# Optimization experiments

Hardware: AMD Instinct MI355X
Metric: run time of the kernel (lower is better)

## Reference

```python
import jax, jax.numpy as jnp
import numpy as np
from jax import lax

STRIDE = 16
ANCHOR_BASE = 16
PRE_NMS = 6000
POST_NMS = 2000
NMS_THRESH = 0.7


def _generate_anchors(base_size=16, ratios=(0.5, 1.0, 2.0), scales=(8, 16, 32)):
    w = h = float(base_size)
    x_ctr = 0.5 * (w - 1)
    y_ctr = 0.5 * (h - 1)
    size = w * h
    anchors = []
    for r in ratios:
        ws = np.round(np.sqrt(size / r))
        hs = np.round(ws * r)
        for s in scales:
            wss, hss = ws * s, hs * s
            anchors.append([x_ctr - 0.5 * (wss - 1), y_ctr - 0.5 * (hss - 1),
                            x_ctr + 0.5 * (wss - 1), y_ctr + 0.5 * (hss - 1)])
    return np.array(anchors, dtype=np.float32)  # [9,4]


def _all_anchors(width, height, stride):
    base = _generate_anchors(ANCHOR_BASE)  # [A,4]
    sx = np.arange(width, dtype=np.float32) * stride
    gy, gx = np.meshgrid(np.arange(height, dtype=np.float32) * stride, sx, indexing='ij')
    shifts = np.stack([gx.ravel(), gy.ravel(), gx.ravel(), gy.ravel()], axis=1)  # [K,4] h-major
    return jnp.asarray((shifts[:, None, :] + base[None, :, :]).reshape(-1, 4))  # [K*A,4]


def setup_inputs() -> dict:
    key = jax.random.key(0)
    k1, k2 = jax.random.split(key)
    H = W = 64
    bbox_deltas = jax.random.normal(k1, (1, 36, H, W), dtype=jnp.float32)
    scores = jax.random.uniform(k2, (1, 2, 9 * H, W), dtype=jnp.float32)
    return {"bbox_deltas": bbox_deltas, "scores": scores, "im_w": 1024, "im_h": 1024}


def reference(bbox_deltas, scores, im_w, im_h):
    H, W = bbox_deltas.shape[2], bbox_deltas.shape[3]
    # fg scores: reshape [1,2,9H,W] -> [1,18,H,W], take channels 9:18
    sc = scores.reshape(1, 18, H, W)[:, 9:, :, :].transpose(0, 2, 3, 1).reshape(-1)
    dl = bbox_deltas.transpose(0, 2, 3, 1).reshape(-1, 4)
    anchors = _all_anchors(W, H, STRIDE)

    # bbox_transform_inv (decode)
    aw = anchors[:, 2] - anchors[:, 0] + 1.0
    ah = anchors[:, 3] - anchors[:, 1] + 1.0
    acx = anchors[:, 0] + 0.5 * aw
    acy = anchors[:, 1] + 0.5 * ah
    pcx = dl[:, 0] * aw + acx
    pcy = dl[:, 1] * ah + acy
    pw = jnp.exp(dl[:, 2]) * aw
    ph = jnp.exp(dl[:, 3]) * ah
    x1 = jnp.clip(pcx - 0.5 * pw, 0.0, im_w - 1.0)
    y1 = jnp.clip(pcy - 0.5 * ph, 0.0, im_h - 1.0)
    x2 = jnp.clip(pcx + 0.5 * pw, 0.0, im_w - 1.0)
    y2 = jnp.clip(pcy + 0.5 * ph, 0.0, im_h - 1.0)
    props = jnp.stack([x1, y1, x2, y2], axis=1)

    # min-size filter
    thresh = 16.0 * (float(im_h) / float(im_w))
    keep_f = ((x2 - x1 + 1.0) >= thresh) & ((y2 - y1 + 1.0) >= thresh)
    sc_m = jnp.where(keep_f, sc, -jnp.inf)

    # pre-NMS top-k by score
    top_sc, idx = lax.top_k(sc_m, PRE_NMS)
    top_p = props[idx]  # [PRE_NMS,4], sorted by score desc
    valid = jnp.isfinite(top_sc)

    # pairwise IoU (with +1 box convention, as in py_cpu_nms)
    bx1, by1, bx2, by2 = top_p[:, 0], top_p[:, 1], top_p[:, 2], top_p[:, 3]
    areas = (bx2 - bx1 + 1.0) * (by2 - by1 + 1.0)
    iw = jnp.maximum(jnp.minimum(bx2[:, None], bx2[None, :]) - jnp.maximum(bx1[:, None], bx1[None, :]) + 1.0, 0.0)
    ih = jnp.maximum(jnp.minimum(by2[:, None], by2[None, :]) - jnp.maximum(by1[:, None], by1[None, :]) + 1.0, 0.0)
    inter = iw * ih
    iou = inter / (areas[:, None] + areas[None, :] - inter)
    sup = iou > NMS_THRESH  # [N,N]

    ar = jnp.arange(PRE_NMS)

    def body(i, keep):
        row = sup[i] & keep[i] & (ar > i)
        return keep & (~row)

    keep = lax.fori_loop(0, PRE_NMS, body, valid)

    # take first POST_NMS kept (in score order), scatter into fixed-size output
    rank = jnp.cumsum(keep.astype(jnp.int32)) - 1
    sel = keep & (rank < POST_NMS)
    dst = jnp.where(sel, rank, POST_NMS)  # invalid rows dumped into slot POST_NMS
    out_b = jnp.zeros((POST_NMS + 1, 4), dtype=jnp.float32).at[dst].set(
        jnp.where(sel[:, None], top_p, 0.0))[:POST_NMS]
    out_s = jnp.zeros((POST_NMS + 1,), dtype=jnp.float32).at[dst].set(
        jnp.where(sel, top_sc, 0.0))[:POST_NMS]
    blob = jnp.concatenate([jnp.zeros((POST_NMS, 1), dtype=jnp.float32), out_b], axis=1)
    return blob, out_s[:, None]
```

## Files before the change

kernel.cpp:

```cpp
#include <hip/hip_runtime.h>
#include <math.h>

typedef unsigned int u32;
typedef unsigned long long u64;

#define NANCH   36864
#define PRE     6000
#define POST    2000
#define NWORDS  94
#define NSTEP   47
#define ROWSP   6016

#define OFF_PROPS   ((size_t)0)
#define OFF_SV      ((size_t)589824)
#define OFF_SORTED  ((size_t)884736)
#define OFF_SEL     ((size_t)932864)
#define OFF_MASKT   ((size_t)1227776)
#define OFF_CTRL    ((size_t)5751808)
#define OFF_H1      ((size_t)5752064)

__device__ __constant__ float BA[9][4] = {
  {-84.f,-40.f,99.f,55.f},   {-176.f,-88.f,191.f,103.f}, {-360.f,-184.f,375.f,199.f},
  {-56.f,-56.f,71.f,71.f},   {-120.f,-120.f,135.f,135.f},{-248.f,-248.f,263.f,263.f},
  {-36.f,-80.f,51.f,95.f},   {-80.f,-168.f,95.f,183.f},  {-168.f,-344.f,183.f,359.f}};

__device__ __forceinline__ u32 key_bin(u32 key) {
  if (key < 0xBF000000u) return 0u;
  u32 b = ((key >> 13) - 0x5F800u) + 1u;
  return b > 1024u ? 1024u : b;
}

__global__ void decode_k(const float* __restrict__ deltas, const float* __restrict__ scores,
                         const int* __restrict__ imw_p, const int* __restrict__ imh_p,
                         float4* __restrict__ props, u64* __restrict__ sortvals,
                         u32* __restrict__ h1, u32* __restrict__ ctrl) {
  #pragma clang fp contract(off)
  if (threadIdx.x == 0) ctrl[6] = 0u;
  int i = blockIdx.x * 256 + threadIdx.x;
  if (i >= NANCH) return;
  int a = i % 9;
  int pix = i / 9;
  int x = pix & 63, y = pix >> 6;

  float sc = scores[(9 + a) * 4096 + pix];
  float d0 = deltas[(a * 4 + 0) * 4096 + pix];
  float d1 = deltas[(a * 4 + 1) * 4096 + pix];
  float d2 = deltas[(a * 4 + 2) * 4096 + pix];
  float d3 = deltas[(a * 4 + 3) * 4096 + pix];

  float gx = (float)(x * 16), gy = (float)(y * 16);
  float ax1 = gx + BA[a][0], ay1 = gy + BA[a][1];
  float ax2 = gx + BA[a][2], ay2 = gy + BA[a][3];
  float aw = ax2 - ax1 + 1.0f, ah = ay2 - ay1 + 1.0f;
  float acx = ax1 + 0.5f * aw, acy = ay1 + 0.5f * ah;

  float pcx = d0 * aw + acx;
  float pcy = d1 * ah + acy;
  float pw = (float)exp((double)d2) * aw;
  float ph = (float)exp((double)d3) * ah;

  float imw1 = (float)imw_p[0] - 1.0f, imh1 = (float)imh_p[0] - 1.0f;
  float x1 = fminf(fmaxf(pcx - 0.5f * pw, 0.0f), imw1);
  float y1 = fminf(fmaxf(pcy - 0.5f * ph, 0.0f), imh1);
  float x2 = fminf(fmaxf(pcx + 0.5f * pw, 0.0f), imw1);
  float y2 = fminf(fmaxf(pcy + 0.5f * ph, 0.0f), imh1);
  props[i] = make_float4(x1, y1, x2, y2);

  float thresh = 16.0f * ((float)imh_p[0] / (float)imw_p[0]);
  bool keep = (x2 - x1 + 1.0f >= thresh) && (y2 - y1 + 1.0f >= thresh);
  u32 key = keep ? (__float_as_uint(sc) | 0x80000000u) : 0u;
  sortvals[i] = ((u64)key << 32) | (u64)(0xFFFFFFFFu - (u32)i);
  u32 bin = key_bin(key);
  if (bin) atomicAdd(&h1[bin], 1u);
}

__global__ void compact_k(const u64* __restrict__ sv, const u32* __restrict__ h1,
                          u32* __restrict__ ctrl, u64* __restrict__ sel) {
  __shared__ u32 Lchosen;
  int t = threadIdx.x;
  if (t < 64) {
    int l = t;
    u32 loc[16], suf[16];
    #pragma unroll
    for (int k = 0; k < 16; ++k) loc[k] = h1[1 + l * 16 + k];
    u32 acc = 0;
    #pragma unroll
    for (int k = 15; k >= 0; --k) { acc += loc[k]; suf[k] = acc; }
    u32 sfx = acc;
    for (int off = 1; off < 64; off <<= 1) {
      u32 o = __shfl_down(sfx, off);
      if (l + off < 64) sfx += o;
    }
    u32 S_above = sfx - acc;
    u64 mball = __ballot(suf[0] + S_above >= (u32)PRE);
    if (mball == 0ULL) { if (l == 0) Lchosen = 0u; }
    else {
      int L = 63 - __builtin_clzll(mball);
      if (l == L) {
        int kk = 0;
        for (int k = 15; k >= 0; --k)
          if (suf[k] + S_above >= (u32)PRE) { kk = k; break; }
        Lchosen = (u32)(1 + 16 * L + kk);
      }
    }
  }
  __syncthreads();
  u32 chosen = Lchosen;
  int i = blockIdx.x * 256 + t;
  if (i >= NANCH) return;
  u64 v = sv[i];
  if (key_bin((u32)(v >> 32)) >= chosen) {
    u32 p = atomicAdd(&ctrl[6], 1u);
    sel[p] = v;
  }
}

__global__ void rank_k(const u64* __restrict__ sel, const u32* __restrict__ ctrl,
                       u64* __restrict__ sorted) {
  __shared__ u64 sj[256];
  u32 n = ctrl[6];
  int i = blockIdx.x * 256 + threadIdx.x;
  if ((u32)(blockIdx.x * 256) >= n) return;
  u64 vi = ((u32)i < n) ? sel[i] : 0ULL;
  u32 cnt = 0;
  for (u32 jb = 0; jb < n; jb += 256) {
    __syncthreads();
    if (jb + threadIdx.x < n) sj[threadIdx.x] = sel[jb + threadIdx.x];
    __syncthreads();
    u32 m = min(256u, n - jb);
    #pragma unroll 8
    for (u32 j = 0; j < m; ++j) cnt += (u32)(sj[j] > vi);
  }
  if ((u32)i < n && cnt < (u32)PRE) sorted[cnt] = vi;
}

__global__ void mask_k(const u64* __restrict__ sorted, const float4* __restrict__ props,
                       u64* __restrict__ maskT) {
  #pragma clang fp contract(off)
  __shared__ float4 cb[64];
  int jb = blockIdx.x;
  if (jb < (int)blockIdx.y) return;
  int i = blockIdx.y * 64 + threadIdx.x;
  int jj = jb * 64 + threadIdx.x;
  float4 cc = make_float4(0.f, 0.f, 0.f, 0.f);
  if (jj < PRE) {
    u64 v = sorted[jj];
    cc = props[0xFFFFu - ((u32)v & 0xFFFFu)];
  }
  cb[threadIdx.x] = cc;
  __syncthreads();
  if (i >= PRE) return;
  u64 vi = sorted[i];
  float4 b = props[0xFFFFu - ((u32)vi & 0xFFFFu)];
  float ai = (b.z - b.x + 1.0f) * (b.w - b.y + 1.0f);
  u64 bits = 0ULL;
  int jmax = min(64, PRE - jb * 64);
  for (int j = 0; j < jmax; ++j) {
    float4 c = cb[j];
    float aj = (c.z - c.x + 1.0f) * (c.w - c.y + 1.0f);
    float iw = fmaxf(fminf(b.z, c.z) - fmaxf(b.x, c.x) + 1.0f, 0.0f);
    float ih = fmaxf(fminf(b.w, c.w) - fmaxf(b.y, c.y) + 1.0f, 0.0f);
    float inter = iw * ih;
    float iou = inter / (ai + aj - inter);
    bits |= ((u64)(iou > 0.7f)) << j;
  }
  maskT[(size_t)jb * ROWSP + i] = bits;
}

__device__ __forceinline__ u64 rl64(u64 v, int lane) {
  u32 lo = (u32)__builtin_amdgcn_readlane((int)(u32)v, lane);
  u32 hi = (u32)__builtin_amdgcn_readlane((int)(u32)(v >> 32), lane);
  return ((u64)hi << 32) | (u64)lo;
}

__global__ void __launch_bounds__(1024) nms_scan_k(const u64* __restrict__ maskT,
                                                   const u64* __restrict__ sorted,
                                                   const float4* __restrict__ props,
                                                   float* __restrict__ out) {
  __shared__ u64 Lrem[NWORDS];
  __shared__ u64 Ldiag[128][2];
  __shared__ u64 Lkb[NWORDS];
  __shared__ u64 LkA, LkB;
  __shared__ int Lstop;
  __shared__ u32 Lpre[NWORDS];
  const int t = threadIdx.x;
  const int g = t >> 7;
  const int w = t & 127;
  const bool loader = (w < NWORDS);
  u64 rv = 0;
  u64 B0[16], B1[16];
  int kept = 0;

#define ISSUE(bb, BUF) \
  if ((bb) < NSTEP && loader) { \
    const u64* p_ = maskT + (size_t)w * ROWSP + (bb) * 128 + g * 16; \
    _Pragma("unroll") \
    for (int k = 0; k < 16; ++k) BUF[k] = p_[k]; \
  }

  ISSUE(0, B0)
  ISSUE(1, B1)

  if (t < NWORDS) { Lrem[t] = 0ULL; Lkb[t] = 0ULL; }
  if (t == 0) Lstop = 0;
  __syncthreads();
  for (int r = t; r < PRE; r += 1024)
    if ((u32)(sorted[r] >> 32) == 0u)
      atomicOr((unsigned long long*)&Lrem[r >> 6], 1ULL << (r & 63));
  if (t == 0)
    atomicOr((unsigned long long*)&Lrem[NWORDS - 1],
             ~((1ULL << (PRE - (NWORDS - 1) * 64)) - 1ULL));
  __syncthreads();

#define STEP(bb, BUF) { \
    const int A_ = 2 * (bb), Bw_ = A_ + 1; \
    if (w == A_ || w == Bw_) {            \
      atomicOr((u32*)&Lrem[w], (u32)rv); \
      atomicOr(((u32*)&Lrem[w]) + 1, (u32)(rv >> 32)); \
      const int c_ = (w == Bw_); \
      _Pragma("unroll") \
      for (int k = 0; k < 16; ++k) { \
        int i_ = g * 16 + k; \
        if (c_ || i_ < 64) Ldiag[i_][c_] = BUF[k]; \
      } \
    } \
    __syncthreads();                      \
    if (t < 64) { \
      u64 a0 = Ldiag[t][0], b0 = Ldiag[t][1], b1 = Ldiag[64 + t][1]; \
      u64 availA = ~Lrem[A_]; \
      u64 availB = ~Lrem[Bw_]; \
      u64 kbA = 0, kbB = 0; \
      while (availA) { \
        int i_ = __builtin_ctzll(availA); \
        kbA |= 1ULL << i_; \
        availA &= ~rl64(a0, i_) & ~((2ULL << i_) - 1ULL);  \
        availB &= ~rl64(b0, i_); \
      } \
      while (availB) { \
        int i_ = __builtin_ctzll(availB); \
        kbB |= 1ULL << i_; \
        availB &= ~rl64(b1, i_) & ~((2ULL << i_) - 1ULL); \
      } \
      if (t == 0) { \
        Lkb[A_] = kbA; Lkb[Bw_] = kbB; LkA = kbA; LkB = kbB; \
        kept += (int)__popcll(kbA) + (int)__popcll(kbB); \
        if (kept >= POST) Lstop = 1; \
      } \
    } \
    __syncthreads();                      \
    { \
      u64 kA_ = LkA, kB_ = LkB; \
      _Pragma("unroll") \
      for (int k = 0; k < 16; ++k) { \
        int i_ = g * 16 + k; \
        u64 bit_ = (i_ < 64) ? (kA_ >> i_) : (kB_ >> (i_ - 64)); \
        rv |= (0ULL - (bit_ & 1ULL)) & BUF[k]; \
      } \
    } \
    ISSUE((bb) + 2, BUF)                  \
    if (Lstop) break; }

  for (int bb = 0; bb < NSTEP; bb += 2) {
    STEP(bb, B0)
    if (bb + 1 < NSTEP) STEP(bb + 1, B1)
  }
#undef ISSUE
#undef STEP

  __syncthreads();
  for (int i = t; i < 12000; i += 1024) out[i] = 0.0f;
  if (t == 0) {
    u32 run = 0;
    for (int w2 = 0; w2 < NWORDS; ++w2) { Lpre[w2] = run; run += (u32)__popcll(Lkb[w2]); }
  }
  __syncthreads();
  for (int i = t; i < PRE; i += 1024) {
    u64 word = Lkb[i >> 6];
    if ((word >> (i & 63)) & 1ULL) {
      u32 rank = Lpre[i >> 6] + (u32)__popcll(word & ((1ULL << (i & 63)) - 1ULL));
      if (rank < POST) {
        u64 v = sorted[i];
        float4 b = props[0xFFFFu - ((u32)v & 0xFFFFu)];
        out[rank * 5 + 1] = b.x;
        out[rank * 5 + 2] = b.y;
        out[rank * 5 + 3] = b.z;
        out[rank * 5 + 4] = b.w;
        out[10000 + rank] = __uint_as_float((u32)(v >> 32) & 0x7FFFFFFFu);
      }
    }
  }
}

extern "C" void kernel_launch(void* const* d_in, const int* in_sizes, int n_in,
                              void* d_out, int out_size, void* d_ws, size_t ws_size,
                              hipStream_t stream) {
  const float* deltas = (const float*)d_in[0];
  const float* scores = (const float*)d_in[1];
  const int* imw = (const int*)d_in[2];
  const int* imh = (const int*)d_in[3];
  char* ws = (char*)d_ws;

  float4* props   = (float4*)(ws + OFF_PROPS);
  u64*    svals   = (u64*)(ws + OFF_SV);
  u64*    sorted  = (u64*)(ws + OFF_SORTED);
  u64*    sel     = (u64*)(ws + OFF_SEL);
  u64*    maskT   = (u64*)(ws + OFF_MASKT);
  u32*    ctrl    = (u32*)(ws + OFF_CTRL);
  u32*    h1      = (u32*)(ws + OFF_H1);

  hipMemsetAsync(h1, 0, 1025 * sizeof(u32), stream);

  decode_k<<<144, 256, 0, stream>>>(deltas, scores, imw, imh, props, svals, h1, ctrl);
  compact_k<<<144, 256, 0, stream>>>(svals, h1, ctrl, sel);
  rank_k<<<144, 256, 0, stream>>>(sel, ctrl, sorted);

  dim3 mgrid(NWORDS, NWORDS);
  mask_k<<<mgrid, 64, 0, stream>>>(sorted, props, maskT);

  nms_scan_k<<<1, 1024, 0, stream>>>(maskT, sorted, props, (float*)d_out);
}
```

Baseline: 378.8 us.

## Restructure NMS scan to one word per step with a single barrier

The serial NMS scan now advances one 64-bit word per step instead of two. Every thread redundantly computes the keep-bits from a double-buffered diagonal block, so the shared broadcast of keep masks and the second barrier per step are gone. The next word's removal mask and diagonal are published by the owning loader thread, and later steps skip loads for words already processed (w >= bb). The trade-off is twice as many steps, each with a barrier, in exchange for fewer barriers per word and no serial single-thread bookkeeping.

```diff
diff --git a/kernel.cpp b/kernel.cpp
--- a/kernel.cpp
+++ b/kernel.cpp
@@ -8,7 +8,6 @@
 #define PRE     6000
 #define POST    2000
 #define NWORDS  94
-#define NSTEP   47
 #define ROWSP   6016
 
 #define OFF_PROPS   ((size_t)0)
@@ -178,31 +177,28 @@
                                                    const float4* __restrict__ props,
                                                    float* __restrict__ out) {
   __shared__ u64 Lrem[NWORDS];
-  __shared__ u64 Ldiag[128][2];
+  __shared__ u64 Ldiag[2][64];
   __shared__ u64 Lkb[NWORDS];
-  __shared__ u64 LkA, LkB;
-  __shared__ int Lstop;
   __shared__ u32 Lpre[NWORDS];
   const int t = threadIdx.x;
   const int g = t >> 7;
   const int w = t & 127;
   const bool loader = (w < NWORDS);
   u64 rv = 0;
-  u64 B0[16], B1[16];
+  u64 B0[8], B1[8];
   int kept = 0;
 
 #define ISSUE(bb, BUF) \
-  if ((bb) < NSTEP && loader) { \
-    const u64* p_ = maskT + (size_t)w * ROWSP + (bb) * 128 + g * 16; \
+  if ((bb) < NWORDS && loader && w >= (bb)) { \
+    const u64* p_ = maskT + (size_t)w * ROWSP + (bb) * 64 + g * 8; \
     _Pragma("unroll") \
-    for (int k = 0; k < 16; ++k) BUF[k] = p_[k]; \
+    for (int k = 0; k < 8; ++k) BUF[k] = p_[k]; \
   }
 
   ISSUE(0, B0)
   ISSUE(1, B1)
 
   if (t < NWORDS) { Lrem[t] = 0ULL; Lkb[t] = 0ULL; }
-  if (t == 0) Lstop = 0;
   __syncthreads();
   for (int r = t; r < PRE; r += 1024)
     if ((u32)(sorted[r] >> 32) == 0u)
@@ -210,59 +206,42 @@
   if (t == 0)
     atomicOr((unsigned long long*)&Lrem[NWORDS - 1],
              ~((1ULL << (PRE - (NWORDS - 1) * 64)) - 1ULL));
-  __syncthreads();
-
-#define STEP(bb, BUF) { \
-    const int A_ = 2 * (bb), Bw_ = A_ + 1; \
-    if (w == A_ || w == Bw_) {            \
-      atomicOr((u32*)&Lrem[w], (u32)rv); \
-      atomicOr(((u32*)&Lrem[w]) + 1, (u32)(rv >> 32)); \
-      const int c_ = (w == Bw_); \
+  if (w == 0) {
+    #pragma unroll
+    for (int k = 0; k < 8; ++k) Ldiag[0][g * 8 + k] = B0[k];
+  }
+  __syncthreads();
+
+#define STEP(bb, BUF, BUFN) { \
+    const int par = (bb) & 1; \
+    u64 dgl = Ldiag[par][t & 63]; \
+    u64 avail = ~Lrem[(bb)]; \
+    u64 kb = 0; \
+    while (avail) { \
+      int i_ = __builtin_ctzll(avail); \
+      kb |= 1ULL << i_; \
+      avail &= ~rl64(dgl, i_) & ~((2ULL << i_) - 1ULL);  \
+    } \
+    kept += (int)__popcll(kb); \
+    if (t == 0) Lkb[(bb)] = kb; \
+    if (loader && w > (bb)) { \
       _Pragma("unroll") \
-      for (int k = 0; k < 16; ++k) { \
-        int i_ = g * 16 + k; \
-        if (c_ || i_ < 64) Ldiag[i_][c_] = BUF[k]; \
-      } \
+      for (int k = 0; k < 8; ++k) \
+        rv |= (0ULL - ((kb >> (g * 8 + k)) & 1ULL)) & BUF[k]; \
     } \
-    __syncthreads();                      \
-    if (t < 64) { \
-      u64 a0 = Ldiag[t][0], b0 = Ldiag[t][1], b1 = Ldiag[64 + t][1]; \
-      u64 availA = ~Lrem[A_]; \
-      u64 availB = ~Lrem[Bw_]; \
-      u64 kbA = 0, kbB = 0; \
-      while (availA) { \
-        int i_ = __builtin_ctzll(availA); \
-        kbA |= 1ULL << i_; \
-        availA &= ~rl64(a0, i_) & ~((2ULL << i_) - 1ULL);  \
-        availB &= ~rl64(b0, i_); \
-      } \
-      while (availB) { \
-        int i_ = __builtin_ctzll(availB); \
-        kbB |= 1ULL << i_; \
-        availB &= ~rl64(b1, i_) & ~((2ULL << i_) - 1ULL); \
-      } \
-      if (t == 0) { \
-        Lkb[A_] = kbA; Lkb[Bw_] = kbB; LkA = kbA; LkB = kbB; \
-        kept += (int)__popcll(kbA) + (int)__popcll(kbB); \
-        if (kept >= POST) Lstop = 1; \
-      } \
+    if ((bb) + 1 < NWORDS && w == (bb) + 1) {    \
+      atomicOr((u32*)&Lrem[(bb) + 1], (u32)rv); \
+      atomicOr(((u32*)&Lrem[(bb) + 1]) + 1, (u32)(rv >> 32)); \
+      _Pragma("unroll") \
+      for (int k = 0; k < 8; ++k) Ldiag[1 - par][g * 8 + k] = BUFN[k]; \
     } \
-    __syncthreads();                      \
-    { \
-      u64 kA_ = LkA, kB_ = LkB; \
-      _Pragma("unroll") \
-      for (int k = 0; k < 16; ++k) { \
-        int i_ = g * 16 + k; \
-        u64 bit_ = (i_ < 64) ? (kA_ >> i_) : (kB_ >> (i_ - 64)); \
-        rv |= (0ULL - (bit_ & 1ULL)) & BUF[k]; \
-      } \
-    } \
-    ISSUE((bb) + 2, BUF)                  \
-    if (Lstop) break; }
-
-  for (int bb = 0; bb < NSTEP; bb += 2) {
-    STEP(bb, B0)
-    if (bb + 1 < NSTEP) STEP(bb + 1, B1)
+    ISSUE((bb) + 2, BUF) \
+    if (kept >= POST) break; \
+    __syncthreads(); }
+
+  for (int bb = 0; bb < NWORDS; bb += 2) {
+    STEP(bb, B0, B1)
+    if (bb + 1 < NWORDS) STEP(bb + 1, B1, B0)
   }
 #undef ISSUE
 #undef STEP
```

After: 344.5 us. 1.1x faster.
